# Kernel tuning notes

Measured on AMD Instinct MI355X. Metric: run time of the kernel, lower is better.

The kernel has to match this reference:

```python
import jax, jax.numpy as jnp
import numpy as np

ENC_DIM = 64

def setup_inputs() -> dict:
    key = jax.random.key(0)
    ks = jax.random.split(key, 7)
    B, C, H, W = 16, 64, 128, 128
    s = 1.0 / np.sqrt(C)
    return {
        "x": jax.random.normal(ks[0], (B, C, H, W), jnp.float32),
        "wq_w": jax.random.normal(ks[1], (ENC_DIM, C), jnp.float32) * s,
        "wq_b": jax.random.normal(ks[2], (ENC_DIM,), jnp.float32) * 0.01,
        "wk_w": jax.random.normal(ks[3], (ENC_DIM, C), jnp.float32) * s,
        "wk_b": jax.random.normal(ks[4], (ENC_DIM,), jnp.float32) * 0.01,
        "wv_w": jax.random.normal(ks[5], (ENC_DIM, C), jnp.float32) * s,
        "wv_b": jax.random.normal(ks[6], (ENC_DIM,), jnp.float32) * 0.01,
    }

def _conv1x1(x, w, b):
    # 1x1 conv == per-pixel linear: [B,C,H,W] x [E,C] -> [B,E,H,W]
    return jnp.einsum('bchw,ec->behw', x, w) + b[None, :, None, None]

def reference(x, wq_w, wq_b, wk_w, wk_b, wv_w, wv_b):
    scaler = jnp.sqrt(jnp.asarray(ENC_DIM, x.dtype))
    Q = _conv1x1(x, wq_w, wq_b)  # [B,E,H,W]
    K = _conv1x1(x, wk_w, wk_b)
    V = _conv1x1(x, wv_w, wv_b)
    # scores = Q @ K^T over last two dims -> [B,E,H,H]
    scores = jnp.einsum('behw,bekw->behk', Q, K) / scaler
    temp1 = jax.nn.softmax(scores, axis=-1)          # softmax over last dim; dropout is identity (eval)
    # Q^T @ K -> [B,E,W,W], softmax over dim -2
    t2 = jnp.einsum('behw,behv->bewv', Q, K) / scaler
    temp2 = jax.nn.softmax(t2, axis=-2)
    # temp1 @ V @ temp2 -> [B,E,H,W]
    tv = jnp.einsum('behk,bekw->behw', temp1, V)
    return jnp.einsum('behw,bewv->behv', tv, temp2)
```

## Files before the change

kernel.cpp:

```cpp
#include <hip/hip_runtime.h>
#include <hip/hip_bf16.h>

typedef __attribute__((ext_vector_type(8))) short short8;
typedef __attribute__((ext_vector_type(4))) float f32x4;

#define MFMA16(a, b, c) __builtin_amdgcn_mfma_f32_16x16x32_bf16((a), (b), (c), 0, 0, 0)

__device__ __forceinline__ short f2bf(float f) {
  union { float f; unsigned u; } v; v.f = f;
  unsigned r = v.u + 0x7fffu + ((v.u >> 16) & 1u);
  return (short)(r >> 16);
}
__device__ __forceinline__ unsigned pack2(float lo, float hi) {
  return (unsigned)(unsigned short)f2bf(lo) | ((unsigned)(unsigned short)f2bf(hi) << 16);
}

__global__ __launch_bounds__(256) void qkv_kernel(
    const float* __restrict__ x,
    const float* __restrict__ wq, const float* __restrict__ bq,
    const float* __restrict__ wk, const float* __restrict__ bk,
    const float* __restrict__ wv, const float* __restrict__ bv,
    short* __restrict__ Q, short* __restrict__ K, short* __restrict__ V)
{
  __shared__ alignas(16) short xs[64 * 256];
  __shared__ alignas(16) short ws[3 * 64 * 64];
  __shared__ float bs[3 * 64];

  const int t    = threadIdx.x;
  const int b    = blockIdx.x >> 6;
  const int pt   = blockIdx.x & 63;
  const int pix0 = pt << 8;
  const float* xb = x + ((size_t)b << 20);

  #pragma unroll
  for (int i = 0; i < 16; ++i) {
    int f4 = i * 256 + t;
    int c  = f4 >> 6;
    int p4 = (f4 & 63) << 2;
    const float4 v = *reinterpret_cast<const float4*>(xb + c * 16384 + pix0 + p4);
    short* d = &xs[c * 256 + p4];
    d[0] = f2bf(v.x); d[1] = f2bf(v.y); d[2] = f2bf(v.z); d[3] = f2bf(v.w);
  }
  {
    #pragma unroll
    for (int i = 0; i < 16; ++i) {
      int idx = i * 256 + t;
      int e = idx >> 6, c = idx & 63;
      int d = e * 64 + (c ^ ((e & 7) << 3));
      ws[d]        = f2bf(wq[idx]);
      ws[d + 4096] = f2bf(wk[idx]);
      ws[d + 8192] = f2bf(wv[idx]);
    }
    if (t < 192) bs[t] = (t < 64) ? bq[t] : ((t < 128) ? bk[t - 64] : bv[t - 128]);
  }
  __syncthreads();

  const int lane = t & 63;
  const int wid  = t >> 6;
  const int p0   = wid << 6;
  const int l15  = lane & 15;
  const int lg   = lane >> 4;

  short8 bfrag[4][2];
  #pragma unroll
  for (int nt = 0; nt < 4; ++nt) {
    int pix = p0 + nt * 16 + l15;
    #pragma unroll
    for (int ks = 0; ks < 2; ++ks) {
      int cb = ks * 32 + (lg << 3);
      short8 f;
      #pragma unroll
      for (int j = 0; j < 8; ++j) f[j] = xs[(cb + j) * 256 + pix];
      bfrag[nt][ks] = f;
    }
  }

  #pragma unroll
  for (int m = 0; m < 3; ++m) {
    short* op = (m == 0) ? Q : ((m == 1) ? K : V);
    short8 afrag[4][2];
    #pragma unroll
    for (int mt = 0; mt < 4; ++mt) {
      int e = mt * 16 + l15;
      #pragma unroll
      for (int ks = 0; ks < 2; ++ks) {
        int cb8 = (ks * 4 + lg) ^ (e & 7);
        afrag[mt][ks] = *reinterpret_cast<const short8*>(&ws[m * 4096 + e * 64 + cb8 * 8]);
      }
    }
    #pragma unroll
    for (int mt = 0; mt < 4; ++mt) {
      #pragma unroll
      for (int nt = 0; nt < 4; ++nt) {
        f32x4 acc = {0.f, 0.f, 0.f, 0.f};
        acc = MFMA16(afrag[mt][0], bfrag[nt][0], acc);
        acc = MFMA16(afrag[mt][1], bfrag[nt][1], acc);
        int e_base = mt * 16 + (lg << 2);
        int pix = pix0 + p0 + nt * 16 + l15;
        #pragma unroll
        for (int r = 0; r < 4; ++r) {
          int e = e_base + r;
          float val = acc[r] + bs[m * 64 + e];
          op[(((size_t)b * 64 + e) << 14) + pix] = f2bf(val);
        }
      }
    }
  }
}

__global__ __launch_bounds__(512) void attn_kernel(
    const short* __restrict__ Qg, const short* __restrict__ Kg,
    const short* __restrict__ Vg, float* __restrict__ out)
{
  __shared__ alignas(16) short B1[128 * 128];
  __shared__ alignas(16) short B2[128 * 128];

  const int t = threadIdx.x;
  const size_t base = (size_t)blockIdx.x << 14;

  auto stage = [&](short* dst, const short* src) {
    #pragma unroll
    for (int i = 0; i < 4; ++i) {
      int eb  = i * 512 + t;
      int row = eb >> 4;
      int cb  = eb & 15;
      float4 v = *reinterpret_cast<const float4*>(src + (eb << 3));
      *reinterpret_cast<float4*>(dst + row * 128 + ((cb ^ (row & 15)) << 3)) = v;
    }
  };

  const int w  = t & 127;
  const int rb = (t >> 7) << 5;

  auto colgather = [&](const short* src, unsigned* p) {
    #pragma unroll
    for (int k2 = 0; k2 < 16; ++k2) {
      int r0 = rb + 2 * k2;
      int r1 = r0 + 1;
      unsigned a  = (unsigned short)src[r0 * 128 + (w ^ ((r0 & 15) << 3))];
      unsigned b_ = (unsigned short)src[r1 * 128 + (w ^ ((r1 & 15) << 3))];
      p[k2] = a | (b_ << 16);
    }
  };
  auto t_write = [&](short* dst, const unsigned* p) {
    const int w15 = w & 15;
    #pragma unroll
    for (int k8 = 0; k8 < 4; ++k8) {
      int hb = (rb >> 3) + k8;
      *reinterpret_cast<short8*>(&dst[w * 128 + ((hb ^ w15) << 3)]) =
          *reinterpret_cast<const short8*>(&p[k8 * 4]);
    }
  };

  const int lane = t & 63;
  const int wid  = t >> 6;
  const int m0   = wid << 4;
  const int l15  = lane & 15;
  const int lg   = lane >> 4;

  f32x4 acc[8];

  auto matmul = [&](const short* bufA, const short* bufB) {
    short8 af[4];
    const short* ba[4];
    #pragma unroll
    for (int ks = 0; ks < 4; ++ks) {
      const int xorb = ((ks * 4 + lg) ^ l15) << 3;
      af[ks] = *reinterpret_cast<const short8*>(&bufA[(m0 + l15) * 128 + xorb]);
      ba[ks] = &bufB[l15 * 128 + xorb];
    }
    #pragma unroll
    for (int n = 0; n < 8; ++n) {
      f32x4 a = {0.f, 0.f, 0.f, 0.f};
      #pragma unroll
      for (int ks = 0; ks < 4; ++ks)
        a = MFMA16(af[ks], *reinterpret_cast<const short8*>(ba[ks] + n * 2048), a);
      acc[n] = a;
    }
  };

  auto softmax_pack = [&](unsigned* pk) {
    #pragma unroll
    for (int r = 0; r < 4; ++r) {
      float mx = acc[0][r];
      #pragma unroll
      for (int n = 1; n < 8; ++n) mx = fmaxf(mx, acc[n][r]);
      mx = fmaxf(mx, __shfl_xor(mx, 1));
      mx = fmaxf(mx, __shfl_xor(mx, 2));
      mx = fmaxf(mx, __shfl_xor(mx, 4));
      mx = fmaxf(mx, __shfl_xor(mx, 8));
      float p[8]; float s = 0.f;
      #pragma unroll
      for (int n = 0; n < 8; ++n) { p[n] = __expf((acc[n][r] - mx) * 0.125f); s += p[n]; }
      s += __shfl_xor(s, 1); s += __shfl_xor(s, 2);
      s += __shfl_xor(s, 4); s += __shfl_xor(s, 8);
      float inv = 1.0f / s;
      #pragma unroll
      for (int np = 0; np < 4; ++np)
        pk[r * 4 + np] = pack2(p[2 * np] * inv, p[2 * np + 1] * inv);
    }
  };

  auto store_pk = [&](short* dst, const unsigned* pk) {
    #pragma unroll
    for (int r = 0; r < 4; ++r) {
      int row = m0 + (lg << 2) + r;
      int sw  = (row & 15) << 3;
      short* dr = dst + row * 128;
      #pragma unroll
      for (int np = 0; np < 4; ++np) {
        unsigned v = pk[r * 4 + np];
        int c0 = (2 * np) * 16 + l15;
        dr[c0 ^ sw]        = (short)(v & 0xffff);
        dr[(c0 + 16) ^ sw] = (short)(v >> 16);
      }
    }
  };

  unsigned t1[16], t2[16];

  stage(B1, Qg + base);
  stage(B2, Kg + base);
  __syncthreads();

  matmul(B1, B2);
  softmax_pack(t1);
  unsigned qc[16], kc[16];
  colgather(B1, qc);
  colgather(B2, kc);
  __syncthreads();

  t_write(B1, qc);
  t_write(B2, kc);
  __syncthreads();

  unsigned vc[16];
  {
    const short* Vsrc = Vg + base;
    #pragma unroll
    for (int k2 = 0; k2 < 16; ++k2) {
      unsigned a  = (unsigned short)Vsrc[(rb + 2 * k2) * 128 + w];
      unsigned b_ = (unsigned short)Vsrc[(rb + 2 * k2 + 1) * 128 + w];
      vc[k2] = a | (b_ << 16);
    }
  }
  matmul(B2, B1);
  softmax_pack(t2);
  __syncthreads();

  t_write(B2, vc);
  store_pk(B1, t1);
  __syncthreads();

  matmul(B1, B2);
  {
    unsigned tv[16];
    #pragma unroll
    for (int r = 0; r < 4; ++r)
      #pragma unroll
      for (int np = 0; np < 4; ++np)
        tv[r * 4 + np] = pack2(acc[2 * np][r], acc[2 * np + 1][r]);
    store_pk(B1, tv);
  }
  __syncthreads();

  store_pk(B2, t2);
  __syncthreads();

  float* ob = out + base;
  #pragma unroll
  for (int n = 0; n < 8; ++n) {
    short8 af[4];
    const short* ba[4];
    #pragma unroll
    for (int ks = 0; ks < 4; ++ks) {
      const int xorb = ((ks * 4 + lg) ^ l15) << 3;
      af[ks] = *reinterpret_cast<const short8*>(&B1[(m0 + l15) * 128 + xorb]);
      ba[ks] = &B2[l15 * 128 + xorb];
    }
    f32x4 a = {0.f, 0.f, 0.f, 0.f};
    #pragma unroll
    for (int ks = 0; ks < 4; ++ks)
      a = MFMA16(af[ks], *reinterpret_cast<const short8*>(ba[ks] + n * 2048), a);
    #pragma unroll
    for (int r = 0; r < 4; ++r) {
      int row = m0 + (lg << 2) + r;
      ob[row * 128 + n * 16 + l15] = a[r];
    }
  }
}

extern "C" void kernel_launch(void* const* d_in, const int* in_sizes, int n_in,
                              void* d_out, int out_size, void* d_ws, size_t ws_size,
                              hipStream_t stream) {
  const float* x  = (const float*)d_in[0];
  const float* wq = (const float*)d_in[1];
  const float* bq = (const float*)d_in[2];
  const float* wk = (const float*)d_in[3];
  const float* bk = (const float*)d_in[4];
  const float* wv = (const float*)d_in[5];
  const float* bv = (const float*)d_in[6];

  const size_t N = (size_t)16 * 64 * 128 * 128;
  short* Q = (short*)d_ws;
  short* K = Q + N;
  short* V = K + N;

  qkv_kernel<<<1024, 256, 0, stream>>>(x, wq, bq, wk, bk, wv, bv, Q, K, V);
  attn_kernel<<<1024, 512, 0, stream>>>(Q, K, V, (float*)d_out);
}
```

Measured before the change: 89.96 us.

## Use four LDS buffers to cut barriers in attention kernel

Grows the attention kernel's shared memory from two 32KB buffers to four (128KB total). Transposed Q and K can then be written to separate buffers while the originals stay live, so three __syncthreads phases are removed and the V load and store_pk writes overlap with the second matmul. It also hoists the A-fragment loads out of the final output loop. The cost is higher LDS use per block, which may limit occupancy to one block per CU.

```diff
diff --git a/kernel.cpp b/kernel.cpp
--- a/kernel.cpp
+++ b/kernel.cpp
@@ -112,8 +112,11 @@
     const short* __restrict__ Qg, const short* __restrict__ Kg,
     const short* __restrict__ Vg, float* __restrict__ out)
 {
-  __shared__ alignas(16) short B1[128 * 128];
-  __shared__ alignas(16) short B2[128 * 128];
+  __shared__ alignas(16) short lds[4 * 16384];
+  short* B1 = lds;
+  short* B2 = lds + 16384;
+  short* B3 = lds + 2 * 16384;
+  short* B4 = lds + 3 * 16384;
 
   const int t = threadIdx.x;
   const size_t base = (size_t)blockIdx.x << 14;
@@ -151,6 +154,14 @@
           *reinterpret_cast<const short8*>(&p[k8 * 4]);
     }
   };
+  auto vload = [&](const short* Vsrc, unsigned* p) {
+    #pragma unroll
+    for (int k2 = 0; k2 < 16; ++k2) {
+      unsigned a  = (unsigned short)Vsrc[(rb + 2 * k2) * 128 + w];
+      unsigned b_ = (unsigned short)Vsrc[(rb + 2 * k2 + 1) * 128 + w];
+      p[k2] = a | (b_ << 16);
+    }
+  };
 
   const int lane = t & 63;
   const int wid  = t >> 6;
@@ -216,8 +227,17 @@
       }
     }
   };
-
-  unsigned t1[16], t2[16];
+  auto store_tv = [&](short* dst) {
+    unsigned tv[16];
+    #pragma unroll
+    for (int r = 0; r < 4; ++r)
+      #pragma unroll
+      for (int np = 0; np < 4; ++np)
+        tv[r * 4 + np] = pack2(acc[2 * np][r], acc[2 * np + 1][r]);
+    store_pk(dst, tv);
+  };
+
+  unsigned t1[16], t2[16], vc[16];
 
   stage(B1, Qg + base);
   stage(B2, Kg + base);
@@ -225,67 +245,51 @@
 
   matmul(B1, B2);
   softmax_pack(t1);
-  unsigned qc[16], kc[16];
-  colgather(B1, qc);
-  colgather(B2, kc);
-  __syncthreads();
-
-  t_write(B1, qc);
-  t_write(B2, kc);
-  __syncthreads();
-
-  unsigned vc[16];
   {
-    const short* Vsrc = Vg + base;
-    #pragma unroll
-    for (int k2 = 0; k2 < 16; ++k2) {
-      unsigned a  = (unsigned short)Vsrc[(rb + 2 * k2) * 128 + w];
-      unsigned b_ = (unsigned short)Vsrc[(rb + 2 * k2 + 1) * 128 + w];
-      vc[k2] = a | (b_ << 16);
-    }
-  }
-  matmul(B2, B1);
+    unsigned qc[16];
+    colgather(B1, qc);
+    t_write(B3, qc);
+  }
+  {
+    unsigned kc[16];
+    colgather(B2, kc);
+    t_write(B4, kc);
+  }
+  vload(Vg + base, vc);
+  __syncthreads();
+
+  store_pk(B1, t1);
+  t_write(B2, vc);
+  matmul(B4, B3);
   softmax_pack(t2);
   __syncthreads();
 
-  t_write(B2, vc);
-  store_pk(B1, t1);
-  __syncthreads();
-
   matmul(B1, B2);
+  store_tv(B1);
+  store_pk(B4, t2);
+  __syncthreads();
+
   {
-    unsigned tv[16];
-    #pragma unroll
-    for (int r = 0; r < 4; ++r)
-      #pragma unroll
-      for (int np = 0; np < 4; ++np)
-        tv[r * 4 + np] = pack2(acc[2 * np][r], acc[2 * np + 1][r]);
-    store_pk(B1, tv);
-  }
-  __syncthreads();
-
-  store_pk(B2, t2);
-  __syncthreads();
-
-  float* ob = out + base;
-  #pragma unroll
-  for (int n = 0; n < 8; ++n) {
+    float* ob = out + base;
     short8 af[4];
     const short* ba[4];
     #pragma unroll
     for (int ks = 0; ks < 4; ++ks) {
       const int xorb = ((ks * 4 + lg) ^ l15) << 3;
       af[ks] = *reinterpret_cast<const short8*>(&B1[(m0 + l15) * 128 + xorb]);
-      ba[ks] = &B2[l15 * 128 + xorb];
-    }
-    f32x4 a = {0.f, 0.f, 0.f, 0.f};
-    #pragma unroll
-    for (int ks = 0; ks < 4; ++ks)
-      a = MFMA16(af[ks], *reinterpret_cast<const short8*>(ba[ks] + n * 2048), a);
-    #pragma unroll
-    for (int r = 0; r < 4; ++r) {
-      int row = m0 + (lg << 2) + r;
-      ob[row * 128 + n * 16 + l15] = a[r];
+      ba[ks] = &B4[l15 * 128 + xorb];
+    }
+    #pragma unroll
+    for (int n = 0; n < 8; ++n) {
+      f32x4 a = {0.f, 0.f, 0.f, 0.f};
+      #pragma unroll
+      for (int ks = 0; ks < 4; ++ks)
+        a = MFMA16(af[ks], *reinterpret_cast<const short8*>(ba[ks] + n * 2048), a);
+      #pragma unroll
+      for (int r = 0; r < 4; ++r) {
+        int row = m0 + (lg << 2) + r;
+        ob[row * 128 + n * 16 + l15] = a[r];
+      }
     }
   }
 }
```

Result: slower. 91.83 us (+2.1%).
